# Kernel optimization log

Hardware: AMD Instinct MI355X
Metric: run time of the kernel (lower is better)

## Reference

```python
import jax, jax.numpy as jnp
import numpy as np

EMBED_DIM = 1024
NUM_HEADS = 16
D_K = EMBED_DIM // NUM_HEADS


def setup_inputs() -> dict:
    key = jax.random.key(0)
    ks = jax.random.split(key, 5)
    x = jax.random.normal(ks[0], (2, 2048, EMBED_DIM), dtype=jnp.float32)
    # kaiming_normal on 2D params: std = sqrt(2/fan_in) with fan_in = in_features
    w_qkv = jax.random.normal(ks[1], (3 * EMBED_DIM, EMBED_DIM), dtype=jnp.float32) * np.sqrt(2.0 / EMBED_DIM)
    b_qkv = jnp.zeros((3 * EMBED_DIM,), dtype=jnp.float32)
    w_o = jax.random.normal(ks[2], (EMBED_DIM, EMBED_DIM), dtype=jnp.float32) * np.sqrt(2.0 / EMBED_DIM)
    b_o = jnp.zeros((EMBED_DIM,), dtype=jnp.float32)
    return {"x": x, "w_qkv": w_qkv, "b_qkv": b_qkv, "w_o": w_o, "b_o": b_o}


def reference(x, w_qkv, b_qkv, w_o, b_o):
    B, N, C = x.shape
    qkv = x @ w_qkv.T + b_qkv  # [B,N,3C]
    q, k, v = jnp.split(qkv, 3, axis=-1)
    # [B,H,N,d_k]
    q = q.reshape(B, N, NUM_HEADS, D_K).transpose(0, 2, 1, 3)
    k = k.reshape(B, N, NUM_HEADS, D_K).transpose(0, 2, 1, 3)
    v = v.reshape(B, N, NUM_HEADS, D_K).transpose(0, 2, 1, 3)
    # NOTE: original forward scales by 1/sqrt(embed_dim), not 1/sqrt(d_k)
    scores = jnp.einsum('bhqd,bhkd->bhqk', q, k) / np.sqrt(C).astype(np.float32)
    causal = jnp.tril(jnp.ones((N, N), dtype=bool))
    scores = jnp.where(causal, scores, -jnp.inf)
    attn = jax.nn.softmax(scores, axis=-1)
    out = jnp.einsum('bhqk,bhkd->bhqd', attn, v)  # [B,H,N,d_k]
    out = out.transpose(0, 2, 1, 3).reshape(B, N, C)
    return out @ w_o.T + b_o
```

## Files before the change

kernel.cpp:

```cpp
#include <hip/hip_runtime.h>
#include <hip/hip_bf16.h>
#include <math.h>

typedef __bf16 bf16_t;
typedef __bf16 bf16x8 __attribute__((ext_vector_type(8)));
typedef __bf16 bf16x4 __attribute__((ext_vector_type(4)));
typedef __bf16 bf16x2 __attribute__((ext_vector_type(2)));
typedef float f32x4 __attribute__((ext_vector_type(4)));
typedef unsigned u32x4 __attribute__((ext_vector_type(4)));

#define SCALE_L2E 0.045084234f
#define ROUND_B 0.0028169f

#define MFMA16(a, b, c) __builtin_amdgcn_mfma_f32_16x16x32_bf16(a, b, c, 0, 0, 0)

__device__ __forceinline__ unsigned pack2(float a, float b) {
  return __builtin_amdgcn_perm(__builtin_bit_cast(unsigned, b),
                               __builtin_bit_cast(unsigned, a), 0x07060302u);
}

__global__ void convert3_f32_bf16(const float* __restrict__ a, int na,
                                  const float* __restrict__ b, int nb,
                                  const float* __restrict__ c, int nc,
                                  bf16_t* __restrict__ oa, bf16_t* __restrict__ ob,
                                  bf16_t* __restrict__ oc) {
  int i = (blockIdx.x * blockDim.x + threadIdx.x) * 8;
  const float* src;
  bf16_t* dst;
  int off;
  if (i < na) { src = a; dst = oa; off = i; }
  else if (i < na + nb) { src = b; dst = ob; off = i - na; }
  else if (i < na + nb + nc) { src = c; dst = oc; off = i - na - nb; }
  else return;
  float4 u = *(const float4*)&src[off];
  float4 v = *(const float4*)&src[off + 4];
  bf16x8 w = {(bf16_t)u.x, (bf16_t)u.y, (bf16_t)u.z, (bf16_t)u.w,
              (bf16_t)v.x, (bf16_t)v.y, (bf16_t)v.z, (bf16_t)v.w};
  *(bf16x8*)&dst[off] = w;
}

#define GLOBAL_AS __attribute__((address_space(1)))
#define LDS_AS __attribute__((address_space(3)))
__device__ __forceinline__ void g2l16(const void* g, void* l) {
  __builtin_amdgcn_global_load_lds((const GLOBAL_AS void*)g, (LDS_AS void*)l,
                                   16, 0, 0);
}

template <typename TC, int BN>
__launch_bounds__(256)
__global__ void gemm_bt_bias(const bf16_t* __restrict__ A,
                             const bf16_t* __restrict__ B,
                             const float* __restrict__ bias,
                             TC* __restrict__ C,
                             int M, int N, int K) {
  constexpr int NT = BN / 32;
  __shared__ bf16_t As[128 * 32];
  __shared__ bf16_t Bs[BN * 32];

  const int t = threadIdx.x;
  const int wave = t >> 6, lane = t & 63, quad = lane >> 4, ln = lane & 15;
  const int wm = (wave >> 1) * 64, wn = (wave & 1) * (BN / 2);
  const int m0 = blockIdx.y * 128, n0 = blockIdx.x * BN;

  const int srow = lane >> 2;
  const int schunk = ((lane & 3) ^ ((lane >> 3) & 3)) * 8;
  const bf16_t* gA0 = &A[(size_t)(m0 + wave * 32 + srow) * K + schunk];
  const bf16_t* gA1 = gA0 + (size_t)16 * K;
  bf16_t* lA0 = &As[(wave * 32) * 32];
  bf16_t* lA1 = &As[(wave * 32 + 16) * 32];
  const bf16_t* gB0 = &B[(size_t)(n0 + (BN == 128 ? wave * 32 : wave * 16) + srow) * K + schunk];
  const bf16_t* gB1 = gB0 + (size_t)16 * K;
  bf16_t* lB0 = &Bs[((BN == 128 ? wave * 32 : wave * 16)) * 32];
  bf16_t* lB1 = &Bs[(wave * 32 + 16) * 32];

  const int cslot = (quad ^ ((ln >> 1) & 3)) * 8;

  f32x4 acc[4][NT];
  for (int i = 0; i < 4; i++)
    for (int j = 0; j < NT; j++) acc[i][j] = (f32x4){0.f, 0.f, 0.f, 0.f};

  for (int k0 = 0; k0 < K; k0 += 32) {
    __syncthreads();
    g2l16(gA0 + k0, lA0);
    g2l16(gA1 + k0, lA1);
    g2l16(gB0 + k0, lB0);
    if (BN == 128) g2l16(gB1 + k0, lB1);
    __syncthreads();

    bf16x8 af[4], bfr[NT];
    for (int mt = 0; mt < 4; mt++)
      af[mt] = *(const bf16x8*)&As[(wm + mt * 16 + ln) * 32 + cslot];
    for (int nt = 0; nt < NT; nt++)
      bfr[nt] = *(const bf16x8*)&Bs[(wn + nt * 16 + ln) * 32 + cslot];
    for (int mt = 0; mt < 4; mt++)
      for (int nt = 0; nt < NT; nt++)
        acc[mt][nt] = MFMA16(af[mt], bfr[nt], acc[mt][nt]);
  }

  for (int nt = 0; nt < NT; nt++) {
    int col = n0 + wn + nt * 16 + ln;
    float bv = bias[col];
    for (int mt = 0; mt < 4; mt++) {
      int row = m0 + wm + mt * 16 + quad * 4;
      for (int r = 0; r < 4; r++)
        C[(size_t)(row + r) * N + col] = (TC)(acc[mt][nt][r] + bv);
    }
  }
}

__launch_bounds__(256, 2)
__global__ void attn_kernel(const bf16_t* __restrict__ qkv,
                            bf16_t* __restrict__ out) {
  constexpr int KP = 72, VP = 72;
  __shared__ __align__(16) bf16_t Ks[64 * KP];
  __shared__ __align__(16) bf16_t Vt[64 * VP];

  const int t = threadIdx.x;
  const int wave = t >> 6, lane = t & 63, quad = lane >> 4, ln = lane & 15;
  const int p = blockIdx.x & 15;
  const int bh = blockIdx.x >> 4;
  const int b = bh >> 4, h = bh & 15;
  const int qA = p * 64, qB = (31 - p) * 64;
  const int itA = p + 1, ntiles = 32 - p;
  const size_t rs = 3072;
  const size_t base = (size_t)b * 2048 * rs;

  const size_t qoffA = base + (size_t)(qA + wave * 16 + ln) * rs + h * 64;
  const size_t qoffB = base + (size_t)(qB + wave * 16 + ln) * rs + h * 64;
  bf16x8 qfA0 = *(const bf16x8*)&qkv[qoffA + quad * 8];
  bf16x8 qfA1 = *(const bf16x8*)&qkv[qoffA + 32 + quad * 8];
  bf16x8 qfB0 = *(const bf16x8*)&qkv[qoffB + quad * 8];
  bf16x8 qfB1 = *(const bf16x8*)&qkv[qoffB + 32 + quad * 8];

  f32x4 oA[4], oB[4];
  float lAx = 0.f, lBx = 0.f;
  for (int ct = 0; ct < 4; ct++) {
    oA[ct] = (f32x4){0.f, 0.f, 0.f, 0.f};
    oB[ct] = (f32x4){0.f, 0.f, 0.f, 0.f};
  }

  const int r0 = t >> 3, c0 = (t & 7) * 8;
  const bf16_t* Kg = &qkv[base + 1024 + h * 64];
  const bf16_t* Vg = &qkv[base + 2048 + h * 64];
  const int ksA = r0 * KP + (((t & 7) + wave) & 7) * 8;
  const int ksB = (r0 + 32) * KP + (((t & 7) + wave + 4) & 7) * 8;
  const int vkoff = ((((r0 >> 2) + (t & 7)) & 7)) * 8 + 2 * (r0 & 3);

  bf16x8 ka = *(const bf16x8*)&Kg[(size_t)r0 * rs + c0];
  bf16x8 kb = *(const bf16x8*)&Kg[(size_t)(r0 + 32) * rs + c0];
  bf16x8 va2 = *(const bf16x8*)&Vg[(size_t)(2 * r0) * rs + c0];
  bf16x8 vb2 = *(const bf16x8*)&Vg[(size_t)(2 * r0 + 1) * rs + c0];

  const int qgA = qA + wave * 16 + ln;
  const int qgB = qB + wave * 16 + ln;

  for (int kt = 0; kt < ntiles; kt++) {
    __syncthreads();
    *(bf16x8*)&Ks[ksA] = ka;
    *(bf16x8*)&Ks[ksB] = kb;
#pragma unroll
    for (int j = 0; j < 8; j++) {
      bf16x2 w2 = {va2[j], vb2[j]};
      *(bf16x2*)&Vt[(c0 + j) * VP + vkoff] = w2;
    }
    __syncthreads();

    if (kt + 1 < ntiles) {
      const size_t nb_ = (size_t)(kt + 1) * 64;
      ka = *(const bf16x8*)&Kg[(nb_ + r0) * rs + c0];
      kb = *(const bf16x8*)&Kg[(nb_ + r0 + 32) * rs + c0];
      va2 = *(const bf16x8*)&Vg[(nb_ + 2 * r0) * rs + c0];
      vb2 = *(const bf16x8*)&Vg[(nb_ + 2 * r0 + 1) * rs + c0];
    }

    const bool doA = (kt < itA);
    const bool dgA = (kt == itA - 1);
    const bool dgB = (kt == ntiles - 1);
    const int kbase = kt * 64;

    bf16x8 BpA[2], BpB[2];
#pragma unroll
    for (int pr = 0; pr < 2; pr++) {
      u32x4 uA, uB;
#pragma unroll
      for (int sh = 0; sh < 2; sh++) {
        const int st = pr * 2 + sh;
        const int krow = st * 16 + ln;
        const int rot = 2 * st + (ln >> 3);
        bf16x8 kf0 = *(const bf16x8*)&Ks[krow * KP + ((quad + rot) & 7) * 8];
        bf16x8 kf1 = *(const bf16x8*)&Ks[krow * KP + ((quad + 4 + rot) & 7) * 8];
        const int k0g = kbase + st * 16 + quad * 4;
        if (doA) {
          f32x4 s = (f32x4){0.f, 0.f, 0.f, 0.f};
          s = MFMA16(kf0, qfA0, s);
          s = MFMA16(kf1, qfA1, s);
          float pv[4];
#pragma unroll
          for (int r = 0; r < 4; r++) {
            float e = __builtin_amdgcn_exp2f(fmaf(s[r], SCALE_L2E, ROUND_B));
            if (dgA && (k0g + r > qgA)) e = 0.f;
            lAx += e;
            pv[r] = e;
          }
          uA[sh * 2]     = pack2(pv[0], pv[1]);
          uA[sh * 2 + 1] = pack2(pv[2], pv[3]);
        }
        {
          f32x4 s = (f32x4){0.f, 0.f, 0.f, 0.f};
          s = MFMA16(kf0, qfB0, s);
          s = MFMA16(kf1, qfB1, s);
          float pv[4];
#pragma unroll
          for (int r = 0; r < 4; r++) {
            float e = __builtin_amdgcn_exp2f(fmaf(s[r], SCALE_L2E, ROUND_B));
            if (dgB && (k0g + r > qgB)) e = 0.f;
            lBx += e;
            pv[r] = e;
          }
          uB[sh * 2]     = pack2(pv[0], pv[1]);
          uB[sh * 2 + 1] = pack2(pv[2], pv[3]);
        }
      }
      BpA[pr] = __builtin_bit_cast(bf16x8, uA);
      BpB[pr] = __builtin_bit_cast(bf16x8, uB);
    }

#pragma unroll
    for (int pr = 0; pr < 2; pr++) {
#pragma unroll
      for (int ct = 0; ct < 4; ct++) {
        const int dd = ct * 16 + ln;
        const int bc = (quad >> 1) + 2 * ct + (ln >> 3);
        const int cA = (4 * pr + bc) & 7;
        const int cB = (4 * pr + 2 + bc) & 7;
        bf16x4 v0 = *(const bf16x4*)&Vt[dd * VP + cA * 8 + (quad & 1) * 4];
        bf16x4 v1 = *(const bf16x4*)&Vt[dd * VP + cB * 8 + (quad & 1) * 4];
        bf16x8 A8 = __builtin_shufflevector(v0, v1, 0, 1, 2, 3, 4, 5, 6, 7);
        if (doA) oA[ct] = MFMA16(A8, BpA[pr], oA[ct]);
        oB[ct] = MFMA16(A8, BpB[pr], oB[ct]);
      }
    }
  }

  lAx += __shfl_xor(lAx, 16);
  lAx += __shfl_xor(lAx, 32);
  lBx += __shfl_xor(lBx, 16);
  lBx += __shfl_xor(lBx, 32);
  const float invA = __builtin_amdgcn_rcpf(lAx);
  const float invB = __builtin_amdgcn_rcpf(lBx);
  const int ocol = h * 64 + quad * 4;
#pragma unroll
  for (int ct = 0; ct < 4; ct++) {
    bf16x4 wa, wb;
#pragma unroll
    for (int r = 0; r < 4; r++) {
      wa[r] = (bf16_t)(oA[ct][r] * invA);
      wb[r] = (bf16_t)(oB[ct][r] * invB);
    }
    *(bf16x4*)&out[(size_t)(b * 2048 + qgA) * 1024 + ocol + ct * 16] = wa;
    *(bf16x4*)&out[(size_t)(b * 2048 + qgB) * 1024 + ocol + ct * 16] = wb;
  }
}

extern "C" void kernel_launch(void* const* d_in, const int* in_sizes, int n_in,
                              void* d_out, int out_size, void* d_ws, size_t ws_size,
                              hipStream_t stream) {
  const float* x     = (const float*)d_in[0];
  const float* w_qkv = (const float*)d_in[1];
  const float* b_qkv = (const float*)d_in[2];
  const float* w_o   = (const float*)d_in[3];
  const float* b_o   = (const float*)d_in[4];
  float* out = (float*)d_out;

  bf16_t* qkv   = (bf16_t*)d_ws;
  bf16_t* xbf   = qkv + (size_t)4096 * 3072;
  bf16_t* wqkvb = xbf + (size_t)4096 * 1024;
  bf16_t* wob   = wqkvb + (size_t)3072 * 1024;
  bf16_t* attn  = xbf;

  const int na = 4096 * 1024, nb = 3072 * 1024, nc = 1024 * 1024;
  convert3_f32_bf16<<<dim3((na + nb + nc) / (256 * 8)), 256, 0, stream>>>(
      x, na, w_qkv, nb, w_o, nc, xbf, wqkvb, wob);

  gemm_bt_bias<bf16_t, 128><<<dim3(3072 / 128, 4096 / 128), 256, 0, stream>>>(
      xbf, wqkvb, b_qkv, qkv, 4096, 3072, 1024);
  attn_kernel<<<dim3(512), 256, 0, stream>>>(qkv, attn);
  gemm_bt_bias<float, 64><<<dim3(1024 / 64, 4096 / 128), 256, 0, stream>>>(
      attn, wob, b_o, out, 4096, 1024, 1024);
}
```

Before: 188.2 us.

## Double-buffer K/V shared tiles and split attention loop into specialized phases

```diff
diff --git a/kernel.cpp b/kernel.cpp
--- a/kernel.cpp
+++ b/kernel.cpp
@@ -112,8 +112,9 @@
 __global__ void attn_kernel(const bf16_t* __restrict__ qkv,
                             bf16_t* __restrict__ out) {
   constexpr int KP = 72, VP = 72;
-  __shared__ __align__(16) bf16_t Ks[64 * KP];
-  __shared__ __align__(16) bf16_t Vt[64 * VP];
+  constexpr int BUF = 64 * KP;
+  __shared__ __align__(16) bf16_t KsB[2 * BUF];
+  __shared__ __align__(16) bf16_t VtB[2 * BUF];
 
   const int t = threadIdx.x;
   const int wave = t >> 6, lane = t & 63, quad = lane >> 4, ln = lane & 15;
@@ -121,7 +122,7 @@
   const int bh = blockIdx.x >> 4;
   const int b = bh >> 4, h = bh & 15;
   const int qA = p * 64, qB = (31 - p) * 64;
-  const int itA = p + 1, ntiles = 32 - p;
+  const int ntiles = 32 - p;
   const size_t rs = 3072;
   const size_t base = (size_t)b * 2048 * rs;
 
@@ -140,91 +141,78 @@
   }
 
   const int r0 = t >> 3, c0 = (t & 7) * 8;
-  const bf16_t* Kg = &qkv[base + 1024 + h * 64];
-  const bf16_t* Vg = &qkv[base + 2048 + h * 64];
   const int ksA = r0 * KP + (((t & 7) + wave) & 7) * 8;
-  const int ksB = (r0 + 32) * KP + (((t & 7) + wave + 4) & 7) * 8;
+  const int ksB2 = (r0 + 32) * KP + (((t & 7) + wave + 4) & 7) * 8;
   const int vkoff = ((((r0 >> 2) + (t & 7)) & 7)) * 8 + 2 * (r0 & 3);
 
-  bf16x8 ka = *(const bf16x8*)&Kg[(size_t)r0 * rs + c0];
-  bf16x8 kb = *(const bf16x8*)&Kg[(size_t)(r0 + 32) * rs + c0];
-  bf16x8 va2 = *(const bf16x8*)&Vg[(size_t)(2 * r0) * rs + c0];
-  bf16x8 vb2 = *(const bf16x8*)&Vg[(size_t)(2 * r0 + 1) * rs + c0];
+  const bf16_t* kpa = &qkv[base + 1024 + h * 64 + (size_t)r0 * rs + c0];
+  const bf16_t* kpb = kpa + (size_t)32 * rs;
+  const bf16_t* vpa = &qkv[base + 2048 + h * 64 + (size_t)(2 * r0) * rs + c0];
+  const bf16_t* vpb = vpa + rs;
+  const size_t tstep = (size_t)64 * rs;
+
+  bf16x8 ka = *(const bf16x8*)kpa; kpa += tstep;
+  bf16x8 kb = *(const bf16x8*)kpb; kpb += tstep;
+  bf16x8 va2 = *(const bf16x8*)vpa; vpa += tstep;
+  bf16x8 vb2 = *(const bf16x8*)vpb; vpb += tstep;
 
   const int qgA = qA + wave * 16 + ln;
   const int qgB = qB + wave * 16 + ln;
 
-  for (int kt = 0; kt < ntiles; kt++) {
-    __syncthreads();
-    *(bf16x8*)&Ks[ksA] = ka;
-    *(bf16x8*)&Ks[ksB] = kb;
+  auto stage_to = [&](int buf) {
+    bf16_t* KsW = &KsB[buf * BUF];
+    bf16_t* VtW = &VtB[buf * BUF];
+    *(bf16x8*)&KsW[ksA] = ka;
+    *(bf16x8*)&KsW[ksB2] = kb;
 #pragma unroll
     for (int j = 0; j < 8; j++) {
       bf16x2 w2 = {va2[j], vb2[j]};
-      *(bf16x2*)&Vt[(c0 + j) * VP + vkoff] = w2;
-    }
-    __syncthreads();
-
-    if (kt + 1 < ntiles) {
-      const size_t nb_ = (size_t)(kt + 1) * 64;
-      ka = *(const bf16x8*)&Kg[(nb_ + r0) * rs + c0];
-      kb = *(const bf16x8*)&Kg[(nb_ + r0 + 32) * rs + c0];
-      va2 = *(const bf16x8*)&Vg[(nb_ + 2 * r0) * rs + c0];
-      vb2 = *(const bf16x8*)&Vg[(nb_ + 2 * r0 + 1) * rs + c0];
-    }
-
-    const bool doA = (kt < itA);
-    const bool dgA = (kt == itA - 1);
-    const bool dgB = (kt == ntiles - 1);
-    const int kbase = kt * 64;
-
-    bf16x8 BpA[2], BpB[2];
+      *(bf16x2*)&VtW[(c0 + j) * VP + vkoff] = w2;
+    }
+  };
+  auto prefetch = [&]() {
+    ka = *(const bf16x8*)kpa; kpa += tstep;
+    kb = *(const bf16x8*)kpb; kpb += tstep;
+    va2 = *(const bf16x8*)vpa; vpa += tstep;
+    vb2 = *(const bf16x8*)vpb; vpb += tstep;
+  };
+  auto load_kfs = [&](const bf16_t* Ks, bf16x8* kf0s, bf16x8* kf1s) {
+#pragma unroll
+    for (int st = 0; st < 4; st++) {
+      const int krow = st * 16 + ln;
+      const int rot = 2 * st + (ln >> 3);
+      kf0s[st] = *(const bf16x8*)&Ks[krow * KP + ((quad + rot) & 7) * 8];
+      kf1s[st] = *(const bf16x8*)&Ks[krow * KP + ((quad + 4 + rot) & 7) * 8];
+    }
+  };
+  auto qk_block = [&](const bf16x8* kf0s, const bf16x8* kf1s, bf16x8 q0,
+                      bf16x8 q1, float& lx, bf16x8* Bp, bool masked,
+                      int kbase, int qg) {
 #pragma unroll
     for (int pr = 0; pr < 2; pr++) {
-      u32x4 uA, uB;
+      u32x4 u;
 #pragma unroll
       for (int sh = 0; sh < 2; sh++) {
         const int st = pr * 2 + sh;
-        const int krow = st * 16 + ln;
-        const int rot = 2 * st + (ln >> 3);
-        bf16x8 kf0 = *(const bf16x8*)&Ks[krow * KP + ((quad + rot) & 7) * 8];
-        bf16x8 kf1 = *(const bf16x8*)&Ks[krow * KP + ((quad + 4 + rot) & 7) * 8];
+        f32x4 s = (f32x4){0.f, 0.f, 0.f, 0.f};
+        s = MFMA16(kf0s[st], q0, s);
+        s = MFMA16(kf1s[st], q1, s);
         const int k0g = kbase + st * 16 + quad * 4;
-        if (doA) {
-          f32x4 s = (f32x4){0.f, 0.f, 0.f, 0.f};
-          s = MFMA16(kf0, qfA0, s);
-          s = MFMA16(kf1, qfA1, s);
-          float pv[4];
-#pragma unroll
-          for (int r = 0; r < 4; r++) {
-            float e = __builtin_amdgcn_exp2f(fmaf(s[r], SCALE_L2E, ROUND_B));
-            if (dgA && (k0g + r > qgA)) e = 0.f;
-            lAx += e;
-            pv[r] = e;
-          }
-          uA[sh * 2]     = pack2(pv[0], pv[1]);
-          uA[sh * 2 + 1] = pack2(pv[2], pv[3]);
+        float pv[4];
+#pragma unroll
+        for (int r = 0; r < 4; r++) {
+          float e = __builtin_amdgcn_exp2f(fmaf(s[r], SCALE_L2E, ROUND_B));
+          if (masked && (k0g + r > qg)) e = 0.f;
+          lx += e;
+          pv[r] = e;
         }
-        {
-          f32x4 s = (f32x4){0.f, 0.f, 0.f, 0.f};
-          s = MFMA16(kf0, qfB0, s);
-          s = MFMA16(kf1, qfB1, s);
-          float pv[4];
-#pragma unroll
-          for (int r = 0; r < 4; r++) {
-            float e = __builtin_amdgcn_exp2f(fmaf(s[r], SCALE_L2E, ROUND_B));
-            if (dgB && (k0g + r > qgB)) e = 0.f;
-            lBx += e;
-            pv[r] = e;
-          }
-          uB[sh * 2]     = pack2(pv[0], pv[1]);
-          uB[sh * 2 + 1] = pack2(pv[2], pv[3]);
-        }
+        u[sh * 2] = pack2(pv[0], pv[1]);
+        u[sh * 2 + 1] = pack2(pv[2], pv[3]);
       }
-      BpA[pr] = __builtin_bit_cast(bf16x8, uA);
-      BpB[pr] = __builtin_bit_cast(bf16x8, uB);
-    }
-
+      Bp[pr] = __builtin_bit_cast(bf16x8, u);
+    }
+  };
+  auto load_vfs = [&](const bf16_t* Vt, bf16x8* A8s) {
 #pragma unroll
     for (int pr = 0; pr < 2; pr++) {
 #pragma unroll
@@ -235,12 +223,44 @@
         const int cB = (4 * pr + 2 + bc) & 7;
         bf16x4 v0 = *(const bf16x4*)&Vt[dd * VP + cA * 8 + (quad & 1) * 4];
         bf16x4 v1 = *(const bf16x4*)&Vt[dd * VP + cB * 8 + (quad & 1) * 4];
-        bf16x8 A8 = __builtin_shufflevector(v0, v1, 0, 1, 2, 3, 4, 5, 6, 7);
-        if (doA) oA[ct] = MFMA16(A8, BpA[pr], oA[ct]);
-        oB[ct] = MFMA16(A8, BpB[pr], oB[ct]);
+        A8s[pr * 4 + ct] = __builtin_shufflevector(v0, v1, 0, 1, 2, 3, 4, 5, 6, 7);
       }
     }
-  }
+  };
+
+  auto body = [&](int kt, bool hasA, bool maskA, bool maskB) {
+    if (kt + 1 < ntiles) {
+      stage_to((kt + 1) & 1);
+      if (kt + 2 < ntiles) prefetch();
+    }
+    const bf16_t* Ks = &KsB[(kt & 1) * BUF];
+    const bf16_t* Vt = &VtB[(kt & 1) * BUF];
+    bf16x8 kf0s[4], kf1s[4];
+    load_kfs(Ks, kf0s, kf1s);
+    bf16x8 BpA[2], BpB[2];
+    if (hasA) qk_block(kf0s, kf1s, qfA0, qfA1, lAx, BpA, maskA, kt * 64, qgA);
+    qk_block(kf0s, kf1s, qfB0, qfB1, lBx, BpB, maskB, kt * 64, qgB);
+    bf16x8 A8s[8];
+    load_vfs(Vt, A8s);
+#pragma unroll
+    for (int pr = 0; pr < 2; pr++) {
+#pragma unroll
+      for (int ct = 0; ct < 4; ct++) {
+        if (hasA) oA[ct] = MFMA16(A8s[pr * 4 + ct], BpA[pr], oA[ct]);
+        oB[ct] = MFMA16(A8s[pr * 4 + ct], BpB[pr], oB[ct]);
+      }
+    }
+    if (kt + 1 < ntiles) __syncthreads();
+  };
+
+  stage_to(0);
+  if (ntiles > 1) prefetch();
+  __syncthreads();
+
+  for (int kt = 0; kt < p; kt++) body(kt, true, false, false);
+  body(p, true, true, false);
+  for (int kt = p + 1; kt < 31 - p; kt++) body(kt, false, false, false);
+  body(31 - p, false, false, true);
 
   lAx += __shfl_xor(lAx, 16);
   lAx += __shfl_xor(lAx, 32);
```

Measured after the change: 179.5 us. 4.6% less time.
